# Kernel tuning notes

Hardware: AMD Instinct MI355X
Metric: run time of the kernel (lower is better)

## Reference

```python
import jax, jax.numpy as jnp
import numpy as np


def setup_inputs() -> dict:
    key = jax.random.key(0)
    ks = jax.random.split(key, 7)
    B, S, I, H, O = 64, 512, 512, 1024, 512
    s_i = 1.0 / np.sqrt(I)
    s_h = 1.0 / np.sqrt(H)
    return {
        "x": jax.random.normal(ks[0], (B, S, I), dtype=jnp.float32),
        "Wi": jax.random.uniform(ks[1], (H, I), jnp.float32, -s_i, s_i),
        "bi": jax.random.uniform(ks[2], (H,), jnp.float32, -s_i, s_i),
        "Wh": jax.random.uniform(ks[3], (H, H), jnp.float32, -s_h, s_h),
        "bh": jax.random.uniform(ks[4], (H,), jnp.float32, -s_h, s_h),
        "Wo": jax.random.uniform(ks[5], (O, H), jnp.float32, -s_h, s_h),
        "bo": jax.random.uniform(ks[6], (O,), jnp.float32, -s_h, s_h),
    }


def reference(x, Wi, bi, Wh, bh, Wo, bo):
    B, S, I = x.shape
    H = Wh.shape[0]
    # Precompute input projections for all timesteps in one big GEMM (same math).
    xi = jnp.einsum("bsi,hi->bsh", x, Wi) + bi + bh  # (B, S, H)

    def step(h, xi_t):
        h_new = jnp.tanh(xi_t + h @ Wh.T)  # (B, H)
        return h_new, h_new

    h0 = jnp.zeros((B, H), dtype=x.dtype)
    h_last, hs = jax.lax.scan(step, h0, jnp.swapaxes(xi, 0, 1))  # hs: (S, B, H)
    # Output projection applied to all hidden states at once.
    outputs = jnp.einsum("sbh,oh->bso", hs, Wo) + bo  # (B, S, O)
    return outputs, h_last
```

## Files before the change

kernel.cpp:

```cpp
#include <hip/hip_runtime.h>
#include <stdint.h>

#define B_ 64
#define S_ 512
#define I_ 512
#define H_ 1024
#define O_ 512
#define HB (B_ * H_)
#define SENT 0x7F80u

typedef __attribute__((ext_vector_type(8))) short bf16x8;
typedef __attribute__((ext_vector_type(4))) float f32x4;
typedef __attribute__((ext_vector_type(2))) unsigned uint32x2;

__device__ inline unsigned short f2bf(float f) {
    union { float f; unsigned u; } v; v.f = f;
    unsigned r = v.u + 0x7fffu + ((v.u >> 16) & 1u);
    return (unsigned short)(r >> 16);
}
__device__ inline float bf2f(unsigned short h) {
    union { unsigned u; float f; } v; v.u = ((unsigned)h) << 16; return v.f;
}


__global__ void k_f2bf4(const float4* __restrict__ src, ushort4* __restrict__ dst, int n4) {
    int i = blockIdx.x * blockDim.x + threadIdx.x;
    if (i < n4) {
        float4 v = src[i];
        ushort4 o;
        o.x = f2bf(v.x); o.y = f2bf(v.y); o.z = f2bf(v.z); o.w = f2bf(v.w);
        dst[i] = o;
    }
}

__global__ void k_init(uint4* __restrict__ hs) {
    size_t i = (size_t)blockIdx.x * blockDim.x + threadIdx.x;
    size_t n = (size_t)(S_ + 1) * HB / 8;
    if (i >= n) return;
    unsigned v = (i < HB / 8) ? 0u : (SENT | (SENT << 16));
    hs[i] = (uint4){v, v, v, v};
}

template <int MODE>
__global__ __launch_bounds__(256) void k_gemm(
    const unsigned short* __restrict__ A, const unsigned short* __restrict__ Bm,
    const float* __restrict__ bias1, const float* __restrict__ bias2,
    void* __restrict__ Cout, int M, int N, int K)
{
    __shared__ unsigned short As[128][40];
    __shared__ unsigned short Bs[128][40];

    const int tid  = threadIdx.x;
    const int m0   = blockIdx.x * 128;
    const int n0   = blockIdx.y * 128;
    const int wave = tid >> 6, lane = tid & 63;
    const int wm   = (wave >> 1) * 64, wn = (wave & 1) * 64;
    const int l16  = lane & 15, q = lane >> 4;

    f32x4 acc[4][4];
#pragma unroll
    for (int a = 0; a < 4; ++a)
#pragma unroll
        for (int b = 0; b < 4; ++b)
            acc[a][b] = (f32x4){0.f, 0.f, 0.f, 0.f};

    for (int k0 = 0; k0 < K; k0 += 32) {
#pragma unroll
        for (int c = 0; c < 2; ++c) {
            int idx = tid + c * 256;
            int row = idx >> 2, col = (idx & 3) * 8;
            if (MODE == 0) {
                *(bf16x8*)&As[row][col] = *(const bf16x8*)&A[(size_t)(m0 + row) * K + k0 + col];
            } else {
                int m = m0 + row, kk = k0 + col;
                int t = m >> 6, b = m & 63;
                size_t E = (size_t)(t + 1) * 65536 + (size_t)(b >> 4) * 16384
                         + (size_t)(kk >> 8) * 4096 + (size_t)((kk >> 5) & 7) * 512
                         + (size_t)((((kk >> 3) & 3) * 16 + (b & 15)) * 8);
                *(bf16x8*)&As[row][col] = *(const bf16x8*)&A[E];
            }
            *(bf16x8*)&Bs[row][col] = *(const bf16x8*)&Bm[(size_t)(n0 + row) * K + k0 + col];
        }
        __syncthreads();

        bf16x8 af[4], bfr[4];
#pragma unroll
        for (int mt = 0; mt < 4; ++mt) af[mt]  = *(const bf16x8*)&As[wm + mt * 16 + l16][q * 8];
#pragma unroll
        for (int nt = 0; nt < 4; ++nt) bfr[nt] = *(const bf16x8*)&Bs[wn + nt * 16 + l16][q * 8];
#pragma unroll
        for (int mt = 0; mt < 4; ++mt)
#pragma unroll
            for (int nt = 0; nt < 4; ++nt)
                acc[mt][nt] = __builtin_amdgcn_mfma_f32_16x16x32_bf16(af[mt], bfr[nt], acc[mt][nt], 0, 0, 0);
        __syncthreads();
    }

#pragma unroll
    for (int mt = 0; mt < 4; ++mt) {
#pragma unroll
        for (int nt = 0; nt < 4; ++nt) {
            int gn = n0 + wn + nt * 16 + l16;
#pragma unroll
            for (int i = 0; i < 4; ++i) {
                int gm = m0 + wm + mt * 16 + q * 4 + i;
                float v = acc[mt][nt][i];
                if (MODE == 0) {
                    v += bias1[gn] + bias2[gn];
                    int bb = gm >> 9, s = gm & (S_ - 1);
                    ((unsigned short*)Cout)[(s * B_ + bb) * H_ + gn] = f2bf(v);
                } else {
                    v += bias1[gn];
                    int t = gm >> 6, bb = gm & (B_ - 1);
                    ((float*)Cout)[((bb << 9) + t) * O_ + gn] = v;
                }
            }
        }
    }
}

__global__ __launch_bounds__(256, 1) void k_scan(
    const unsigned short* __restrict__ xi,
    const unsigned short* __restrict__ Wh,
    unsigned short* __restrict__ hs)
{
    __shared__ f32x4 part[2][4][4][64];

    const int bid = blockIdx.x;
    const int g   = bid & 3;
    const int j   = bid >> 2;
    const int n0  = j * 64;
    const int r0  = g * 16;
    const int tid = threadIdx.x;
    const int wave = tid >> 6, lane = tid & 63;
    const int l16 = lane & 15, q = lane >> 4;
    const int kbase = wave * 256;

    bf16x8 wreg[4][8];
#pragma unroll
    for (int n = 0; n < 4; ++n)
#pragma unroll
        for (int ks = 0; ks < 8; ++ks)
            wreg[n][ks] = *(const bf16x8*)&Wh[(size_t)(n0 + n * 16 + l16) * H_ + kbase + ks * 32 + q * 8];

    const size_t wavebase = (size_t)g * 16384 + (size_t)wave * 4096;

    const int c_rel = tid >> 7;
    const int u  = (tid >> 1) & 63;
    const int qo = u >> 4, qq = (u >> 2) & 3, ii = u & 3;
    const int nn = (c_rel << 1) | (qo >> 1);
    const int lb = (qq << 4) | ((qo & 1) << 3) | ((tid & 1) << 2);
    const int row  = qq * 4 + ii;
    const int colb = n0 + nn * 16 + ((qo & 1) << 3) + ((tid & 1) << 2);
    const size_t regbase = (size_t)g * 16384 + (size_t)(j >> 2) * 4096
                         + (size_t)(j & 3) * 1024;

    const unsigned short* xip = xi + (size_t)(r0 + row) * H_ + colb;
    uint32x2 xv = *(const uint32x2*)xip;

    for (int t = 0; t < S_; ++t) {
        const char* hb = (const char*)hs + 2 * ((size_t)t * 65536 + wavebase);
        uint4 hv[8];
        for (;;) {
#pragma unroll
            for (int k = 0; k < 8; ++k) {
                const char* a = hb + (size_t)(k * 64 + lane) * 16;
                asm volatile("global_load_dwordx4 %0, %1, off sc0 sc1"
                             : "=v"(hv[k]) : "v"(a));
            }
            asm volatile("s_waitcnt vmcnt(0)" ::: "memory");
            __builtin_amdgcn_sched_barrier(0);
            unsigned acc_or = 0;
#pragma unroll
            for (int k = 0; k < 8; ++k)
                acc_or |= (hv[k].x | hv[k].y) | (hv[k].z | hv[k].w);
            if (__ballot((acc_or & 0x40004000u) != 0u) == 0ull) break;
        }

        uint32x2 xv_next = *(const uint32x2*)(xip + (size_t)(t + 1) * HB);

        f32x4 acc[4];
#pragma unroll
        for (int n = 0; n < 4; ++n) acc[n] = (f32x4){0.f, 0.f, 0.f, 0.f};
#pragma unroll
        for (int ks = 0; ks < 8; ++ks) {
            bf16x8 av = __builtin_bit_cast(bf16x8, hv[ks]);
#pragma unroll
            for (int n = 0; n < 4; ++n)
                acc[n] = __builtin_amdgcn_mfma_f32_16x16x32_bf16(av, wreg[n][ks], acc[n], 0, 0, 0);
        }

        const int p = t & 1;
#pragma unroll
        for (int n = 0; n < 4; ++n)
            part[p][wave][n][lane] = acc[n];
        __syncthreads();

        float s2[4] = {0.f, 0.f, 0.f, 0.f};
#pragma unroll
        for (int ws = 0; ws < 4; ++ws) {
            const float* pp = (const float*)&part[p][ws][nn][lb];
#pragma unroll
            for (int c = 0; c < 4; ++c)
                s2[c] += pp[((c ^ qq) << 2) + ii];
        }
        const bool b0 = (qq & 1) != 0, b1 = (qq & 2) != 0;
        float t0 = b0 ? s2[1] : s2[0], t1 = b0 ? s2[0] : s2[1];
        float t2 = b0 ? s2[3] : s2[2], t3 = b0 ? s2[2] : s2[3];
        float e0 = b1 ? t2 : t0, e1 = b1 ? t3 : t1;
        float e2 = b1 ? t0 : t2, e3 = b1 ? t1 : t3;
        float s[4] = { e0, e1, e2, e3 };

        float xf[4] = { bf2f((unsigned short)(xv[0] & 0xffffu)),
                        bf2f((unsigned short)(xv[0] >> 16)),
                        bf2f((unsigned short)(xv[1] & 0xffffu)),
                        bf2f((unsigned short)(xv[1] >> 16)) };
        unsigned short h16[4];
#pragma unroll
        for (int c = 0; c < 4; ++c) {
            float x = s[c] + xf[c];
            float e = __expf(2.f * x);
            h16[c] = f2bf(1.f - 2.f / (e + 1.f));
        }
        uint32x2 val;
        val[0] = (unsigned)h16[0] | ((unsigned)h16[1] << 16);
        val[1] = (unsigned)h16[2] | ((unsigned)h16[3] << 16);
        const unsigned short* ap = hs + (size_t)(t + 1) * 65536 + regbase + (size_t)tid * 4;
        asm volatile("global_store_dwordx2 %0, %1, off sc0 sc1"
                     :: "v"(ap), "v"(val) : "memory");

        xv = xv_next;
    }
}

__global__ void k_hlast(const unsigned short* __restrict__ hsT, float* __restrict__ out) {
    int i = blockIdx.x * blockDim.x + threadIdx.x;
    if (i >= HB) return;
    int b = i >> 10, kk = i & 1023;
    size_t E = (size_t)S_ * 65536 + (size_t)(b >> 4) * 16384
             + (size_t)(kk >> 8) * 4096 + (size_t)((kk >> 5) & 7) * 512
             + (size_t)((((kk >> 3) & 3) * 16 + (b & 15)) * 8) + (kk & 7);
    out[i] = bf2f(hsT[E]);
}

extern "C" void kernel_launch(void* const* d_in, const int* in_sizes, int n_in,
                              void* d_out, int out_size, void* d_ws, size_t ws_size,
                              hipStream_t stream) {
    const float* x  = (const float*)d_in[0];
    const float* Wi = (const float*)d_in[1];
    const float* bi = (const float*)d_in[2];
    const float* Wh = (const float*)d_in[3];
    const float* bh = (const float*)d_in[4];
    const float* Wo = (const float*)d_in[5];
    const float* bo = (const float*)d_in[6];
    float* out = (float*)d_out;

    char* p = (char*)d_ws;
    unsigned short* x_bf  = (unsigned short*)p; p += (size_t)B_ * S_ * I_ * 2;
    unsigned short* Wi_bf = (unsigned short*)p; p += (size_t)H_ * I_ * 2;
    unsigned short* Wh_bf = (unsigned short*)p; p += (size_t)H_ * H_ * 2;
    unsigned short* Wo_bf = (unsigned short*)p; p += (size_t)O_ * H_ * 2;
    unsigned short* xi    = (unsigned short*)p; p += (size_t)S_ * B_ * H_ * 2;
    unsigned short* hs    = (unsigned short*)p; p += (size_t)(S_ + 1) * HB * 2;

    int n4;
    n4 = B_ * S_ * I_ / 4;
    k_f2bf4<<<(n4 + 255) / 256, 256, 0, stream>>>((const float4*)x,  (ushort4*)x_bf,  n4);
    n4 = H_ * I_ / 4;
    k_f2bf4<<<(n4 + 255) / 256, 256, 0, stream>>>((const float4*)Wi, (ushort4*)Wi_bf, n4);
    n4 = H_ * H_ / 4;
    k_f2bf4<<<(n4 + 255) / 256, 256, 0, stream>>>((const float4*)Wh, (ushort4*)Wh_bf, n4);
    n4 = O_ * H_ / 4;
    k_f2bf4<<<(n4 + 255) / 256, 256, 0, stream>>>((const float4*)Wo, (ushort4*)Wo_bf, n4);

    {
        size_t n = (size_t)(S_ + 1) * HB / 8;
        k_init<<<(unsigned)((n + 255) / 256), 256, 0, stream>>>((uint4*)hs);
    }

    k_gemm<0><<<dim3(B_ * S_ / 128, H_ / 128), 256, 0, stream>>>(
        x_bf, Wi_bf, bi, bh, (void*)xi, B_ * S_, H_, I_);

    k_scan<<<64, 256, 0, stream>>>(xi, Wh_bf, hs);

    k_gemm<1><<<dim3(B_ * S_ / 128, O_ / 128), 256, 0, stream>>>(
        hs, Wo_bf, bo, nullptr, (void*)out, B_ * S_, O_, H_);

    k_hlast<<<(HB + 255) / 256, 256, 0, stream>>>(hs, out + (size_t)B_ * S_ * O_);
}
```

Measured before the change: 974.0 us.

## Double-buffer spin-poll loads of hidden state and use a lighter barrier

The scan's spin-wait on the previous step's hidden state now keeps two sets of eight loads in flight, alternating between them. While one set is checked for sentinel values the other is already being fetched, so poll latency overlaps. The __syncthreads is replaced with an explicit lgkmcnt wait plus s_barrier, which avoids waiting on outstanding vector memory loads. This adds register pressure from a second 8x uint4 buffer and relies on hand-written waitcnt values, which is fragile, and leftover in-flight loads carry across iterations.

```diff
diff --git a/kernel.cpp b/kernel.cpp
--- a/kernel.cpp
+++ b/kernel.cpp
@@ -119,6 +119,31 @@
     }
 }
 
+#define ISSUE8(SET)                                                   \
+    _Pragma("unroll")                                                 \
+    for (int k = 0; k < 8; ++k) {                                     \
+        const char* a = hb + (size_t)(k * 64 + lane) * 16;            \
+        asm volatile("global_load_dwordx4 %0, %1, off sc0 sc1"        \
+                     : "=v"(SET[k]) : "v"(a));                        \
+    }
+#define CHECK8(SET, OK)                                               \
+    {                                                                 \
+        unsigned o_ = 0;                                              \
+        _Pragma("unroll")                                             \
+        for (int k = 0; k < 8; ++k)                                   \
+            o_ |= (SET[k].x | SET[k].y) | (SET[k].z | SET[k].w);      \
+        OK = (__ballot((o_ & 0x40004000u) != 0u) == 0ull);            \
+    }
+#define MFMA8(SET)                                                    \
+    _Pragma("unroll")                                                 \
+    for (int ks = 0; ks < 8; ++ks) {                                  \
+        bf16x8 av = __builtin_bit_cast(bf16x8, SET[ks]);              \
+        _Pragma("unroll")                                             \
+        for (int n = 0; n < 4; ++n)                                   \
+            acc[n] = __builtin_amdgcn_mfma_f32_16x16x32_bf16(         \
+                av, wreg[n][ks], acc[n], 0, 0, 0);                    \
+    }
+
 __global__ __launch_bounds__(256, 1) void k_scan(
     const unsigned short* __restrict__ xi,
     const unsigned short* __restrict__ Wh,
@@ -160,21 +185,26 @@
 
     for (int t = 0; t < S_; ++t) {
         const char* hb = (const char*)hs + 2 * ((size_t)t * 65536 + wavebase);
-        uint4 hv[8];
+
+        asm volatile("s_waitcnt vmcnt(2)" ::: "memory");
+        __builtin_amdgcn_sched_barrier(0);
+
+        uint4 hvA[8], hvB[8];
+        ISSUE8(hvA)
+        ISSUE8(hvB)
+        bool useA;
         for (;;) {
-#pragma unroll
-            for (int k = 0; k < 8; ++k) {
-                const char* a = hb + (size_t)(k * 64 + lane) * 16;
-                asm volatile("global_load_dwordx4 %0, %1, off sc0 sc1"
-                             : "=v"(hv[k]) : "v"(a));
-            }
-            asm volatile("s_waitcnt vmcnt(0)" ::: "memory");
+            bool ok;
+            asm volatile("s_waitcnt vmcnt(8)" ::: "memory");
             __builtin_amdgcn_sched_barrier(0);
-            unsigned acc_or = 0;
-#pragma unroll
-            for (int k = 0; k < 8; ++k)
-                acc_or |= (hv[k].x | hv[k].y) | (hv[k].z | hv[k].w);
-            if (__ballot((acc_or & 0x40004000u) != 0u) == 0ull) break;
+            CHECK8(hvA, ok)
+            if (ok) { useA = true; break; }
+            ISSUE8(hvA)
+            asm volatile("s_waitcnt vmcnt(8)" ::: "memory");
+            __builtin_amdgcn_sched_barrier(0);
+            CHECK8(hvB, ok)
+            if (ok) { useA = false; break; }
+            ISSUE8(hvB)
         }
 
         uint32x2 xv_next = *(const uint32x2*)(xip + (size_t)(t + 1) * HB);
@@ -182,19 +212,15 @@
         f32x4 acc[4];
 #pragma unroll
         for (int n = 0; n < 4; ++n) acc[n] = (f32x4){0.f, 0.f, 0.f, 0.f};
-#pragma unroll
-        for (int ks = 0; ks < 8; ++ks) {
-            bf16x8 av = __builtin_bit_cast(bf16x8, hv[ks]);
-#pragma unroll
-            for (int n = 0; n < 4; ++n)
-                acc[n] = __builtin_amdgcn_mfma_f32_16x16x32_bf16(av, wreg[n][ks], acc[n], 0, 0, 0);
-        }
+        if (useA) { MFMA8(hvA) } else { MFMA8(hvB) }
 
         const int p = t & 1;
 #pragma unroll
         for (int n = 0; n < 4; ++n)
             part[p][wave][n][lane] = acc[n];
-        __syncthreads();
+        asm volatile("s_waitcnt lgkmcnt(0)" ::: "memory");
+        __builtin_amdgcn_s_barrier();
+        __builtin_amdgcn_sched_barrier(0);
 
         float s2[4] = {0.f, 0.f, 0.f, 0.f};
 #pragma unroll
```

Measured after the change: 1.115 ms. 14.5% more time.
